# Kernel optimization log

Measured on AMD Instinct MI355X. Metric: run time of the kernel, lower is better.

The kernel has to match this reference:

```python
import jax, jax.numpy as jnp
import numpy as np

B, N, S = 8, 4096, 1024          # clouds, points per cloud, fps samples per cloud
C_IN = 64
R_LIST = (0.1, 0.2, 0.4)
K_LIST = (16, 32, 64)
CHANNELS = ([C_IN + 3, 64, 64, 128], [C_IN + 3, 128, 128, 256], [C_IN + 3, 128, 128, 256])


def setup_inputs() -> dict:
    key = jax.random.key(0)
    ks = jax.random.split(key, 2 + 9)
    inp = {}
    inp["x"] = jax.random.normal(ks[0], (B * N, C_IN), jnp.float32)
    inp["pos"] = jax.random.uniform(ks[1], (B * N, 3), jnp.float32)
    inp["batch"] = jnp.repeat(jnp.arange(B, dtype=jnp.int32), N)
    ki = 2
    for s, ch in enumerate(CHANNELS):
        for l in range(len(ch) - 1):
            inp[f"W{s}_{l}"] = jax.random.normal(ks[ki], (ch[l], ch[l + 1]), jnp.float32) / np.float32(np.sqrt(ch[l]))
            inp[f"b{s}_{l}"] = jnp.zeros((ch[l + 1],), jnp.float32)
        ki += 1
    return inp


def _fps_one(pos_b):
    """Farthest point sampling on one cloud [N,3] -> [S] int32 indices (start at 0)."""
    def step(carry, _):
        min_d, last = carry
        d = jnp.sum((pos_b - pos_b[last]) ** 2, axis=-1)          # [N]
        min_d = jnp.minimum(min_d, d)
        return (min_d, jnp.argmax(min_d).astype(jnp.int32)), last
    init = (jnp.full((N,), jnp.inf, pos_b.dtype), jnp.int32(0))
    _, idx = jax.lax.scan(step, init, None, length=S)
    return idx


def _scale(xb, posb, centers, r, K, Ws, bs):
    """Radius ball query (K nearest within r) + PointConv (MLP on [x_j, pos_j-pos_i], max-aggr)."""
    d2 = jnp.sum((centers[:, None, :] - posb[None, :, :]) ** 2, axis=-1)  # [S,N]
    neg = jnp.where(d2 <= r * r, -d2, -jnp.inf)
    vals, nbr = jax.lax.top_k(neg, K)                                      # [S,K]
    valid = vals > -jnp.inf                                                # center itself always valid
    feat = jnp.concatenate([xb[nbr], posb[nbr] - centers[:, None, :]], axis=-1)  # [S,K,C+3]
    h = feat
    for W, b in zip(Ws, bs):
        h = jax.nn.relu(h @ W + b)
    h = jnp.where(valid[..., None], h, -jnp.inf)
    return jnp.max(h, axis=1)                                              # [S,out]


def _forward(x, pos, batch, params):
    xb = x.reshape(B, N, C_IN)
    posb = pos.reshape(B, N, 3)
    idx = jax.vmap(_fps_one)(posb)                                # [B,S]
    centers = jnp.take_along_axis(posb, idx[..., None], axis=1)   # [B,S,3]
    outs = []
    for s in range(3):
        Ws, bs = params[s]
        f = lambda xb_, pb_, c_, Ws=Ws, bs=bs, s=s: _scale(xb_, pb_, c_, R_LIST[s], K_LIST[s], Ws, bs)
        outs.append(jax.vmap(f)(xb, posb, centers))
    new_x = jnp.concatenate(outs, axis=-1).reshape(B * S, -1)     # [B*S, 640]
    new_pos = centers.reshape(B * S, 3)
    new_batch = jnp.repeat(jnp.arange(B, dtype=batch.dtype), S)
    return new_x, new_pos, new_batch


def reference(x, pos, batch, W0_0, b0_0, W0_1, b0_1, W0_2, b0_2,
              W1_0, b1_0, W1_1, b1_1, W1_2, b1_2,
              W2_0, b2_0, W2_1, b2_1, W2_2, b2_2):
    params = (((W0_0, W0_1, W0_2), (b0_0, b0_1, b0_2)),
              ((W1_0, W1_1, W1_2), (b1_0, b1_1, b1_2)),
              ((W2_0, W2_1, W2_2), (b2_0, b2_1, b2_2)))
    return _forward(x, pos, batch, params)
```

## Files before the change

### kernel.cpp

```cpp
#include <hip/hip_runtime.h>

#define NB 8
#define NP 4096
#define NS 1024
#define PROGSTRIDE 32

typedef _Float16 f16x8 __attribute__((ext_vector_type(8)));
typedef _Float16 f16x4 __attribute__((ext_vector_type(4)));
typedef float f32x4 __attribute__((ext_vector_type(4)));

#define DPP_MAX(v, ctrl)                                                     \
    v = fmaxf(v, __int_as_float(__builtin_amdgcn_update_dpp(                 \
                __float_as_int(v), __float_as_int(v), (ctrl), 0xf, 0xf, false)))

struct PrepArgs {
    const float* src[9];
    _Float16* dst[9];
    int kr[9], kp[9], nc[9];
};

template <int K>
__device__ __forceinline__ void select_center(
        const float* __restrict__ pb,
        const float* __restrict__ centers,
        int* __restrict__ nbr, int* __restrict__ nvalid,
        float r2, int scid) {
#pragma clang fp contract(off)
    const int lane = threadIdx.x & 63;
    const unsigned kr2 = __float_as_uint(r2);
    const float cx = centers[scid * 3 + 0];
    const float cy = centers[scid * 3 + 1];
    const float cz = centers[scid * 3 + 2];

    unsigned key[64];
#pragma unroll
    for (int i = 0; i < 64; ++i) {
        const float* pp = pb + (size_t)(lane + i * 64) * 3;
        float dx = pp[0] - cx; float sx = dx * dx;
        float dy = pp[1] - cy; float sy = dy * dy;
        float dz = pp[2] - cz; float sz = dz * dz;
        float d2 = sx + sy; d2 = d2 + sz;
        key[i] = __float_as_uint(d2);
    }

    const unsigned long long below = (1ull << lane) - 1ull;
    int c_cnt = 0;
#pragma unroll
    for (int i = 0; i < 64; ++i)
        c_cnt += __popcll(__ballot(key[i] <= kr2));

    unsigned thr = kr2;
    int nv = c_cnt;
    bool need_ties = false;
    unsigned tkey = 0;
    if (c_cnt > K) {
        nv = K;
        unsigned lo = 0, hi = kr2;
        need_ties = true;
        while (lo < hi) {
            unsigned mid = lo + ((hi - lo) >> 1);
            int cnt = 0;
#pragma unroll
            for (int i = 0; i < 64; ++i)
                cnt += __popcll(__ballot(key[i] <= mid));
            if (cnt == K) { thr = mid; need_ties = false; break; }
            if (cnt > K) hi = mid; else lo = mid + 1;
        }
        tkey = lo;
    }

    if (!need_ties) {
        int base = 0;
#pragma unroll
        for (int i = 0; i < 64; ++i) {
            unsigned long long m = __ballot(key[i] <= thr);
            if (key[i] <= thr)
                nbr[(size_t)scid * K + base + __popcll(m & below)] = lane + i * 64;
            base += __popcll(m);
        }
    } else {
        const unsigned t = tkey;
        int m_cnt = 0;
#pragma unroll
        for (int i = 0; i < 64; ++i)
            m_cnt += __popcll(__ballot(key[i] < t));
        const int rem = K - m_cnt;
        int base = 0, tcnt = 0;
#pragma unroll
        for (int i = 0; i < 64; ++i) {
            unsigned long long lt = __ballot(key[i] < t);
            unsigned long long eq = __ballot(key[i] == t);
            if (key[i] < t) {
                nbr[(size_t)scid * K + base + __popcll(lt & below)] = lane + i * 64;
            } else if (key[i] == t) {
                int tr = tcnt + __popcll(eq & below);
                if (tr < rem) nbr[(size_t)scid * K + (m_cnt + tr)] = lane + i * 64;
            }
            base += __popcll(lt);
            tcnt += __popcll(eq);
        }
    }
    if (lane == 0) nvalid[scid] = nv;
}

__global__ __launch_bounds__(512, 1) void fps_select_fused(
        const float* __restrict__ pos,
        float* __restrict__ centers,
        float* __restrict__ out_pos,
        float* __restrict__ out_batch,
        int* __restrict__ nbr0, int* __restrict__ nbr1, int* __restrict__ nbr2,
        int* __restrict__ nval,
        unsigned* __restrict__ prog,
        PrepArgs pa) {
#pragma clang fp contract(off)
    const int tid = threadIdx.x;
    const int lane = tid & 63;

    if (blockIdx.x < NB) {
        const int b = blockIdx.x;
        const int wid = tid >> 6;
        __shared__ float4 slot[2][8];

        const float* pb = pos + (size_t)b * NP * 3;
        float px[8], py[8], pz[8], md[8];
        {
            const float4* pv = (const float4*)(pb + tid * 24);
            float4 q0 = pv[0], q1 = pv[1], q2 = pv[2];
            float4 q3 = pv[3], q4 = pv[4], q5 = pv[5];
            px[0] = q0.x; py[0] = q0.y; pz[0] = q0.z;
            px[1] = q0.w; py[1] = q1.x; pz[1] = q1.y;
            px[2] = q1.z; py[2] = q1.w; pz[2] = q2.x;
            px[3] = q2.y; py[3] = q2.z; pz[3] = q2.w;
            px[4] = q3.x; py[4] = q3.y; pz[4] = q3.z;
            px[5] = q3.w; py[5] = q4.x; pz[5] = q4.y;
            px[6] = q4.z; py[6] = q4.w; pz[6] = q5.x;
            px[7] = q5.y; py[7] = q5.z; pz[7] = q5.w;
        }
#pragma unroll
        for (int j = 0; j < 8; ++j) md[j] = __builtin_inff();
        for (int t = tid; t < NS; t += 512) out_batch[b * NS + t] = (float)b;

        float cx = pb[0], cy = pb[1], cz = pb[2];
        if (tid == 0) {
            size_t o = (size_t)(b * NS) * 3;
            centers[o + 0] = cx; centers[o + 1] = cy; centers[o + 2] = cz;
            out_pos[o + 0] = cx; out_pos[o + 1] = cy; out_pos[o + 2] = cz;
        }

        int par = 0;
        for (int t = 1; t < NS; ++t) {
            float bv = -1.0f, bx = cx, by = cy, bz = cz;
#pragma unroll
            for (int j = 0; j < 8; ++j) {
                float dx = px[j] - cx; float sx = dx * dx;
                float dy = py[j] - cy; float sy = dy * dy;
                float dz = pz[j] - cz; float sz = dz * dz;
                float d = sx + sy; d = d + sz;
                float m = fminf(md[j], d);
                md[j] = m;
                bool c = m > bv;
                bv = c ? m : bv;
                bx = c ? px[j] : bx;
                by = c ? py[j] : by;
                bz = c ? pz[j] : bz;
            }
            float v = bv;
            DPP_MAX(v, 0x111);
            DPP_MAX(v, 0x112);
            DPP_MAX(v, 0x114);
            DPP_MAX(v, 0x118);
            DPP_MAX(v, 0x142);
            DPP_MAX(v, 0x143);
            const float mx = __int_as_float(
                __builtin_amdgcn_readlane(__float_as_int(v), 63));
            unsigned long long tie = __ballot(bv == mx);
            if (lane == __ffsll(tie) - 1)
                slot[par][wid] = make_float4(mx, bx, by, bz);
            __syncthreads();
            float4 s0 = slot[par][0], s1 = slot[par][1];
            float4 s2 = slot[par][2], s3 = slot[par][3];
            float4 s4 = slot[par][4], s5 = slot[par][5];
            float4 s6 = slot[par][6], s7 = slot[par][7];
            float4 a01 = (s1.x > s0.x) ? s1 : s0;
            float4 a23 = (s3.x > s2.x) ? s3 : s2;
            float4 a45 = (s5.x > s4.x) ? s5 : s4;
            float4 a67 = (s7.x > s6.x) ? s7 : s6;
            float4 b03 = (a23.x > a01.x) ? a23 : a01;
            float4 b47 = (a67.x > a45.x) ? a67 : a45;
            float4 wn = (b47.x > b03.x) ? b47 : b03;
            cx = wn.y; cy = wn.z; cz = wn.w;
            if (tid == 0) {
                size_t o = (size_t)(b * NS + t) * 3;
                centers[o + 0] = cx; centers[o + 1] = cy; centers[o + 2] = cz;
                out_pos[o + 0] = cx; out_pos[o + 1] = cy; out_pos[o + 2] = cz;
                if ((t & 15) == 15)
                    __hip_atomic_store(&prog[b * PROGSTRIDE], (unsigned)(t + 1),
                                       __ATOMIC_RELEASE, __HIP_MEMORY_SCOPE_AGENT);
            }
            par ^= 1;
        }
    } else {
        const int wblk = blockIdx.x - NB;
        {
            const int wtid = wblk * 512 + tid;
            const int NW = 248 * 512;
#pragma unroll 1
            for (int m = 0; m < 9; ++m) {
                const int kp = pa.kp[m], kr = pa.kr[m], nc = pa.nc[m];
                const float* src = pa.src[m];
                _Float16* dst = pa.dst[m];
                const int tot = kp * nc;
                for (int i = wtid; i < tot; i += NW) {
                    int n = i / kp, k = i - n * kp;
                    dst[i] = (k < kr) ? (_Float16)src[(size_t)k * nc + n]
                                      : (_Float16)0.f;
                }
            }
        }
        const int wid = tid >> 6;
        const int wave_id = wblk * 8 + wid;
        const int NWAVE = 248 * 8;
        const int NTASK = 3 * NB * NS;
        for (int T = wave_id; T < NTASK; T += NWAVE) {
            const int s = T / 24;
            const int r = T - s * 24;
            const int b = r & 7;
            const int seg = r >> 3;
            const int scid = b * NS + s;
            while (__hip_atomic_load(&prog[b * PROGSTRIDE], __ATOMIC_ACQUIRE,
                                     __HIP_MEMORY_SCOPE_AGENT) <= (unsigned)s)
                __builtin_amdgcn_s_sleep(32);
            const float* pb = pos + (size_t)b * NP * 3;
            if (seg == 0)
                select_center<16>(pb, centers, nbr0, nval,
                                  (float)(0.1 * 0.1), scid);
            else if (seg == 1)
                select_center<32>(pb, centers, nbr1, nval + 8192,
                                  (float)(0.2 * 0.2), scid);
            else
                select_center<64>(pb, centers, nbr2, nval + 16384,
                                  (float)(0.4 * 0.4), scid);
        }
    }
}

template <int M, int C1, int C2, int C3, int OFF, int NCTR>
__device__ void mlp_body(
        char* smem,
        const float* __restrict__ x, const float* __restrict__ pos,
        const float* __restrict__ centers,
        const int* __restrict__ nbr, const int* __restrict__ nvalid,
        const _Float16* __restrict__ wt1, const _Float16* __restrict__ wt2,
        const _Float16* __restrict__ wt3,
        const float* __restrict__ b1, const float* __restrict__ b2,
        const float* __restrict__ b3,
        float* __restrict__ out, int blk) {
    constexpr int K1P = 96;
    constexpr int S1 = K1P + 8;
    constexpr int S2 = C1 + 8;
    constexpr int S3 = C2 + 8;
    constexpr int MT = M / 16;
    constexpr int NCH1 = C1 / 4, NCH2 = C2 / 4, NCH3 = C3 / 4;
    constexpr int NT1 = NCH1 / 16, NT2 = NCH2 / 16, NT3 = NCH3 / 16;
    constexpr int KT1 = K1P / 32, KT2 = C1 / 32, KT3 = C2 / 32;

    _Float16* feat = (_Float16*)smem;
    _Float16* h1 = feat + M * S1;
    _Float16* h2 = h1 + M * S2;
    int* outmax = (int*)(h2 + M * S3);

    const int tid = threadIdx.x;
    const int lane = tid & 63;
    const int w = tid >> 6;
    const int lm = lane & 15;
    const int lq = lane >> 4;

    f16x8 wf1[NT1][KT1], wf2[NT2][KT2], wf3[NT3][KT3];
    float bb1[NT1], bb2[NT2], bb3[NT3];
#pragma unroll
    for (int nt = 0; nt < NT1; ++nt) {
        int n = w * NCH1 + nt * 16 + lm;
        bb1[nt] = b1[n];
#pragma unroll
        for (int kt = 0; kt < KT1; ++kt)
            wf1[nt][kt] = *(const f16x8*)(wt1 + (size_t)n * K1P + kt * 32 + lq * 8);
    }
#pragma unroll
    for (int nt = 0; nt < NT2; ++nt) {
        int n = w * NCH2 + nt * 16 + lm;
        bb2[nt] = b2[n];
#pragma unroll
        for (int kt = 0; kt < KT2; ++kt)
            wf2[nt][kt] = *(const f16x8*)(wt2 + (size_t)n * C1 + kt * 32 + lq * 8);
    }
#pragma unroll
    for (int nt = 0; nt < NT3; ++nt) {
        int n = w * NCH3 + nt * 16 + lm;
        bb3[nt] = b3[n];
#pragma unroll
        for (int kt = 0; kt < KT3; ++kt)
            wf3[nt][kt] = *(const f16x8*)(wt3 + (size_t)n * C2 + kt * 32 + lq * 8);
    }

    for (int cc = 0; cc < NCTR; ++cc) {
        const int cid = blk * NCTR + cc;
        const int bidx = cid >> 10;
        const int nv = nvalid[cid];
        const float cx = centers[cid * 3 + 0];
        const float cy = centers[cid * 3 + 1];
        const float cz = centers[cid * 3 + 2];
        for (int i = tid; i < C3; i += 256) outmax[i] = 0;

#pragma unroll
        for (int it = tid; it < M * 16; it += 256) {
            const int r = it >> 4, sub = it & 15;
            if (r < nv) {
                int pt = nbr[(size_t)cid * M + r];
                float4 v = *(const float4*)(x + ((size_t)(bidx * NP) + pt) * 64 + sub * 4);
                f16x4 hv = {(_Float16)v.x, (_Float16)v.y, (_Float16)v.z, (_Float16)v.w};
                *(f16x4*)(feat + r * S1 + sub * 4) = hv;
            }
        }
#pragma unroll
        for (int it = tid; it < M * 4; it += 256) {
            const int r = it >> 2, q = it & 3;
            f16x8 z = {(_Float16)0.f, (_Float16)0.f, (_Float16)0.f, (_Float16)0.f,
                       (_Float16)0.f, (_Float16)0.f, (_Float16)0.f, (_Float16)0.f};
            if (q == 0 && r < nv) {
                int pt = nbr[(size_t)cid * M + r];
                const float* pr = pos + ((size_t)(bidx * NP) + pt) * 3;
                z[0] = (_Float16)(pr[0] - cx);
                z[1] = (_Float16)(pr[1] - cy);
                z[2] = (_Float16)(pr[2] - cz);
            }
            *(f16x8*)(feat + r * S1 + 64 + q * 8) = z;
        }
        __syncthreads();

#pragma unroll
        for (int mt = 0; mt < MT; ++mt) {
            f16x8 a[KT1];
#pragma unroll
            for (int kt = 0; kt < KT1; ++kt)
                a[kt] = *(const f16x8*)(feat + (mt * 16 + lm) * S1 + kt * 32 + lq * 8);
#pragma unroll
            for (int nt = 0; nt < NT1; ++nt) {
                f32x4 acc = {bb1[nt], bb1[nt], bb1[nt], bb1[nt]};
#pragma unroll
                for (int kt = 0; kt < KT1; ++kt)
                    acc = __builtin_amdgcn_mfma_f32_16x16x32_f16(a[kt], wf1[nt][kt], acc, 0, 0, 0);
                const int gc = w * NCH1 + nt * 16 + lm;
#pragma unroll
                for (int rg = 0; rg < 4; ++rg)
                    h1[(mt * 16 + lq * 4 + rg) * S2 + gc] = (_Float16)fmaxf(acc[rg], 0.f);
            }
        }
        __syncthreads();

#pragma unroll
        for (int mt = 0; mt < MT; ++mt) {
            f16x8 a[KT2];
#pragma unroll
            for (int kt = 0; kt < KT2; ++kt)
                a[kt] = *(const f16x8*)(h1 + (mt * 16 + lm) * S2 + kt * 32 + lq * 8);
#pragma unroll
            for (int nt = 0; nt < NT2; ++nt) {
                f32x4 acc = {bb2[nt], bb2[nt], bb2[nt], bb2[nt]};
#pragma unroll
                for (int kt = 0; kt < KT2; ++kt)
                    acc = __builtin_amdgcn_mfma_f32_16x16x32_f16(a[kt], wf2[nt][kt], acc, 0, 0, 0);
                const int gc = w * NCH2 + nt * 16 + lm;
#pragma unroll
                for (int rg = 0; rg < 4; ++rg)
                    h2[(mt * 16 + lq * 4 + rg) * S3 + gc] = (_Float16)fmaxf(acc[rg], 0.f);
            }
        }
        __syncthreads();

#pragma unroll
        for (int mt = 0; mt < MT; ++mt) {
            f16x8 a[KT3];
#pragma unroll
            for (int kt = 0; kt < KT3; ++kt)
                a[kt] = *(const f16x8*)(h2 + (mt * 16 + lm) * S3 + kt * 32 + lq * 8);
#pragma unroll
            for (int nt = 0; nt < NT3; ++nt) {
                f32x4 acc = {bb3[nt], bb3[nt], bb3[nt], bb3[nt]};
#pragma unroll
                for (int kt = 0; kt < KT3; ++kt)
                    acc = __builtin_amdgcn_mfma_f32_16x16x32_f16(a[kt], wf3[nt][kt], acc, 0, 0, 0);
                float mx = -1.f;
#pragma unroll
                for (int rg = 0; rg < 4; ++rg) {
                    int row = mt * 16 + lq * 4 + rg;
                    float v = fmaxf(acc[rg], 0.f);
                    if (row < nv) mx = fmaxf(mx, v);
                }
                mx = fmaxf(mx, __shfl_xor(mx, 16));
                mx = fmaxf(mx, __shfl_xor(mx, 32));
                if (lane < 16)
                    atomicMax(&outmax[w * NCH3 + nt * 16 + lm], __float_as_int(mx));
            }
        }
        __syncthreads();
        for (int i = tid; i < C3; i += 256)
            out[(size_t)cid * 640 + OFF + i] = __int_as_float(outmax[i]);
        __syncthreads();
    }
}

struct MlpW {
    const _Float16* w[9];
    const float* bias[9];
};

__global__ __launch_bounds__(256, 2) void mlp_all(
        const float* __restrict__ x, const float* __restrict__ pos,
        const float* __restrict__ centers,
        const int* __restrict__ nbr0, const int* __restrict__ nbr1,
        const int* __restrict__ nbr2, const int* __restrict__ nval,
        MlpW ww, float* __restrict__ out) {
    extern __shared__ char smem[];
    const int blk = blockIdx.x;
    if (blk < 1024)
        mlp_body<16, 64, 64, 128, 0, 8>(smem, x, pos, centers, nbr0, nval,
            ww.w[0], ww.w[1], ww.w[2], ww.bias[0], ww.bias[1], ww.bias[2], out, blk);
    else if (blk < 2048)
        mlp_body<32, 128, 128, 256, 128, 8>(smem, x, pos, centers, nbr1, nval + 8192,
            ww.w[3], ww.w[4], ww.w[5], ww.bias[3], ww.bias[4], ww.bias[5], out, blk - 1024);
    else
        mlp_body<64, 128, 128, 256, 384, 8>(smem, x, pos, centers, nbr2, nval + 16384,
            ww.w[6], ww.w[7], ww.w[8], ww.bias[6], ww.bias[7], ww.bias[8], out, blk - 2048);
}

extern "C" void kernel_launch(void* const* d_in, const int* in_sizes, int n_in,
                              void* d_out, int out_size, void* d_ws, size_t ws_size,
                              hipStream_t stream) {
    const float* x = (const float*)d_in[0];
    const float* pos = (const float*)d_in[1];
    const float* W0_0 = (const float*)d_in[3];
    const float* b0_0 = (const float*)d_in[4];
    const float* W0_1 = (const float*)d_in[5];
    const float* b0_1 = (const float*)d_in[6];
    const float* W0_2 = (const float*)d_in[7];
    const float* b0_2 = (const float*)d_in[8];
    const float* W1_0 = (const float*)d_in[9];
    const float* b1_0 = (const float*)d_in[10];
    const float* W1_1 = (const float*)d_in[11];
    const float* b1_1 = (const float*)d_in[12];
    const float* W1_2 = (const float*)d_in[13];
    const float* b1_2 = (const float*)d_in[14];
    const float* W2_0 = (const float*)d_in[15];
    const float* b2_0 = (const float*)d_in[16];
    const float* W2_1 = (const float*)d_in[17];
    const float* b2_1 = (const float*)d_in[18];
    const float* W2_2 = (const float*)d_in[19];
    const float* b2_2 = (const float*)d_in[20];

    float* out = (float*)d_out;
    char* ws = (char*)d_ws;
    float* centers = (float*)(ws + 0);
    int* nbr0 = (int*)(ws + 98304);
    int* nbr1 = (int*)(ws + 622592);
    int* nbr2 = (int*)(ws + 1671168);
    int* nval = (int*)(ws + 3768320);
    _Float16* w0t1 = (_Float16*)(ws + 3866624);
    _Float16* w0t2 = (_Float16*)(ws + 3878912);
    _Float16* w0t3 = (_Float16*)(ws + 3887104);
    _Float16* w1t1 = (_Float16*)(ws + 3903488);
    _Float16* w1t2 = (_Float16*)(ws + 3928064);
    _Float16* w1t3 = (_Float16*)(ws + 3960832);
    _Float16* w2t1 = (_Float16*)(ws + 4026368);
    _Float16* w2t2 = (_Float16*)(ws + 4050944);
    _Float16* w2t3 = (_Float16*)(ws + 4083712);
    unsigned* prog = (unsigned*)(ws + 4149248);

    float* out_pos = out + (size_t)8192 * 640;
    float* out_batch = out_pos + (size_t)8192 * 3;

    hipMemsetAsync(prog, 0, NB * PROGSTRIDE * sizeof(unsigned), stream);

    PrepArgs pa;
    pa.src[0] = W0_0; pa.dst[0] = w0t1; pa.kr[0] = 67;  pa.kp[0] = 96;  pa.nc[0] = 64;
    pa.src[1] = W0_1; pa.dst[1] = w0t2; pa.kr[1] = 64;  pa.kp[1] = 64;  pa.nc[1] = 64;
    pa.src[2] = W0_2; pa.dst[2] = w0t3; pa.kr[2] = 64;  pa.kp[2] = 64;  pa.nc[2] = 128;
    pa.src[3] = W1_0; pa.dst[3] = w1t1; pa.kr[3] = 67;  pa.kp[3] = 96;  pa.nc[3] = 128;
    pa.src[4] = W1_1; pa.dst[4] = w1t2; pa.kr[4] = 128; pa.kp[4] = 128; pa.nc[4] = 128;
    pa.src[5] = W1_2; pa.dst[5] = w1t3; pa.kr[5] = 128; pa.kp[5] = 128; pa.nc[5] = 256;
    pa.src[6] = W2_0; pa.dst[6] = w2t1; pa.kr[6] = 67;  pa.kp[6] = 96;  pa.nc[6] = 128;
    pa.src[7] = W2_1; pa.dst[7] = w2t2; pa.kr[7] = 128; pa.kp[7] = 128; pa.nc[7] = 128;
    pa.src[8] = W2_2; pa.dst[8] = w2t3; pa.kr[8] = 128; pa.kp[8] = 128; pa.nc[8] = 256;

    fps_select_fused<<<dim3(256), dim3(512), 0, stream>>>(
        pos, centers, out_pos, out_batch, nbr0, nbr1, nbr2, nval, prog, pa);

    MlpW ww;
    ww.w[0] = w0t1; ww.w[1] = w0t2; ww.w[2] = w0t3;
    ww.w[3] = w1t1; ww.w[4] = w1t2; ww.w[5] = w1t3;
    ww.w[6] = w2t1; ww.w[7] = w2t2; ww.w[8] = w2t3;
    ww.bias[0] = b0_0; ww.bias[1] = b0_1; ww.bias[2] = b0_2;
    ww.bias[3] = b1_0; ww.bias[4] = b1_1; ww.bias[5] = b1_2;
    ww.bias[6] = b2_0; ww.bias[7] = b2_1; ww.bias[8] = b2_2;

    mlp_all<<<dim3(3072), dim3(256), 49152, stream>>>(
        x, pos, centers, nbr0, nbr1, nbr2, nval, ww, out);
}
```

Baseline: 1.119 ms.

## Fuse MLP into persistent FPS kernel with per-unit readiness counters

Merges the separate MLP kernel into the persistent FPS/ball-query kernel. Blocks are now split three ways: 8 run FPS, 120 run neighbour selection, and 128 run the MLP. The MLP blocks take 8-center units from a global atomic queue and wait on a per-unit ready counter that the selection waves increment with release semantics. The goal is to overlap MLP compute with the serial FPS tail instead of running it afterwards. In exchange, the MLP now runs on far fewer blocks with 512 threads, and half the waves sit idle in the smallest scale. Every MLP block also redoes the weight transpose into fp16, and spin-waiting adds latency.

```diff
diff --git a/kernel.cpp b/kernel.cpp
--- a/kernel.cpp
+++ b/kernel.cpp
@@ -4,6 +4,8 @@
 #define NP 4096
 #define NS 1024
 #define PROGSTRIDE 32
+#define SELB 120
+#define NUNIT 3072
 
 typedef _Float16 f16x8 __attribute__((ext_vector_type(8)));
 typedef _Float16 f16x4 __attribute__((ext_vector_type(4)));
@@ -17,6 +19,11 @@
     const float* src[9];
     _Float16* dst[9];
     int kr[9], kp[9], nc[9];
+};
+
+struct MlpW {
+    const _Float16* w[9];
+    const float* bias[9];
 };
 
 template <int K>
@@ -103,7 +110,179 @@
     if (lane == 0) nvalid[scid] = nv;
 }
 
-__global__ __launch_bounds__(512, 1) void fps_select_fused(
+template <int M, int C1, int C2, int C3, int OFF, int AW>
+__device__ void mlp_unit(
+        char* smem,
+        const float* __restrict__ x, const float* __restrict__ pos,
+        const float* __restrict__ centers,
+        const int* __restrict__ nbr, const int* __restrict__ nvalid,
+        const _Float16* __restrict__ wt1, const _Float16* __restrict__ wt2,
+        const _Float16* __restrict__ wt3,
+        const float* __restrict__ b1, const float* __restrict__ b2,
+        const float* __restrict__ b3,
+        float* __restrict__ out, int cid0) {
+    constexpr int K1P = 96;
+    constexpr int S1 = K1P + 8;
+    constexpr int S2 = C1 + 8;
+    constexpr int S3 = C2 + 8;
+    constexpr int MT = M / 16;
+    constexpr int NCH1 = C1 / AW, NCH2 = C2 / AW, NCH3 = C3 / AW;
+    constexpr int NT1 = NCH1 / 16, NT2 = NCH2 / 16, NT3 = NCH3 / 16;
+    constexpr int KT1 = K1P / 32, KT2 = C1 / 32, KT3 = C2 / 32;
+
+    _Float16* feat = (_Float16*)smem;
+    _Float16* h1 = feat + M * S1;
+    _Float16* h2 = h1 + M * S2;
+    int* outmax = (int*)(h2 + M * S3);
+
+    const int tid = threadIdx.x;
+    const int lane = tid & 63;
+    const int w = tid >> 6;
+    const int lm = lane & 15;
+    const int lq = lane >> 4;
+    const bool act = (w < AW);
+
+    f16x8 wf1[NT1][KT1], wf2[NT2][KT2], wf3[NT3][KT3];
+    float bb1[NT1], bb2[NT2], bb3[NT3];
+    if (act) {
+#pragma unroll
+        for (int nt = 0; nt < NT1; ++nt) {
+            int n = w * NCH1 + nt * 16 + lm;
+            bb1[nt] = b1[n];
+#pragma unroll
+            for (int kt = 0; kt < KT1; ++kt)
+                wf1[nt][kt] = *(const f16x8*)(wt1 + (size_t)n * K1P + kt * 32 + lq * 8);
+        }
+#pragma unroll
+        for (int nt = 0; nt < NT2; ++nt) {
+            int n = w * NCH2 + nt * 16 + lm;
+            bb2[nt] = b2[n];
+#pragma unroll
+            for (int kt = 0; kt < KT2; ++kt)
+                wf2[nt][kt] = *(const f16x8*)(wt2 + (size_t)n * C1 + kt * 32 + lq * 8);
+        }
+#pragma unroll
+        for (int nt = 0; nt < NT3; ++nt) {
+            int n = w * NCH3 + nt * 16 + lm;
+            bb3[nt] = b3[n];
+#pragma unroll
+            for (int kt = 0; kt < KT3; ++kt)
+                wf3[nt][kt] = *(const f16x8*)(wt3 + (size_t)n * C2 + kt * 32 + lq * 8);
+        }
+    }
+
+    for (int cc = 0; cc < 8; ++cc) {
+        const int cid = cid0 + cc;
+        const int bidx = cid >> 10;
+        const int nv = nvalid[cid];
+        const float cx = centers[cid * 3 + 0];
+        const float cy = centers[cid * 3 + 1];
+        const float cz = centers[cid * 3 + 2];
+        for (int i = tid; i < C3; i += 512) outmax[i] = 0;
+
+        for (int it = tid; it < M * 16; it += 512) {
+            const int r = it >> 4, sub = it & 15;
+            if (r < nv) {
+                int pt = nbr[(size_t)cid * M + r];
+                float4 v = *(const float4*)(x + ((size_t)(bidx * NP) + pt) * 64 + sub * 4);
+                f16x4 hv = {(_Float16)v.x, (_Float16)v.y, (_Float16)v.z, (_Float16)v.w};
+                *(f16x4*)(feat + r * S1 + sub * 4) = hv;
+            }
+        }
+        for (int it = tid; it < M * 4; it += 512) {
+            const int r = it >> 2, q = it & 3;
+            f16x8 z = {(_Float16)0.f, (_Float16)0.f, (_Float16)0.f, (_Float16)0.f,
+                       (_Float16)0.f, (_Float16)0.f, (_Float16)0.f, (_Float16)0.f};
+            if (q == 0 && r < nv) {
+                int pt = nbr[(size_t)cid * M + r];
+                const float* pr = pos + ((size_t)(bidx * NP) + pt) * 3;
+                z[0] = (_Float16)(pr[0] - cx);
+                z[1] = (_Float16)(pr[1] - cy);
+                z[2] = (_Float16)(pr[2] - cz);
+            }
+            *(f16x8*)(feat + r * S1 + 64 + q * 8) = z;
+        }
+        __syncthreads();
+
+        if (act) {
+#pragma unroll
+            for (int mt = 0; mt < MT; ++mt) {
+                f16x8 a[KT1];
+#pragma unroll
+                for (int kt = 0; kt < KT1; ++kt)
+                    a[kt] = *(const f16x8*)(feat + (mt * 16 + lm) * S1 + kt * 32 + lq * 8);
+#pragma unroll
+                for (int nt = 0; nt < NT1; ++nt) {
+                    f32x4 acc = {bb1[nt], bb1[nt], bb1[nt], bb1[nt]};
+#pragma unroll
+                    for (int kt = 0; kt < KT1; ++kt)
+                        acc = __builtin_amdgcn_mfma_f32_16x16x32_f16(a[kt], wf1[nt][kt], acc, 0, 0, 0);
+                    const int gc = w * NCH1 + nt * 16 + lm;
+#pragma unroll
+                    for (int rg = 0; rg < 4; ++rg)
+                        h1[(mt * 16 + lq * 4 + rg) * S2 + gc] = (_Float16)fmaxf(acc[rg], 0.f);
+                }
+            }
+        }
+        __syncthreads();
+
+        if (act) {
+#pragma unroll
+            for (int mt = 0; mt < MT; ++mt) {
+                f16x8 a[KT2];
+#pragma unroll
+                for (int kt = 0; kt < KT2; ++kt)
+                    a[kt] = *(const f16x8*)(h1 + (mt * 16 + lm) * S2 + kt * 32 + lq * 8);
+#pragma unroll
+                for (int nt = 0; nt < NT2; ++nt) {
+                    f32x4 acc = {bb2[nt], bb2[nt], bb2[nt], bb2[nt]};
+#pragma unroll
+                    for (int kt = 0; kt < KT2; ++kt)
+                        acc = __builtin_amdgcn_mfma_f32_16x16x32_f16(a[kt], wf2[nt][kt], acc, 0, 0, 0);
+                    const int gc = w * NCH2 + nt * 16 + lm;
+#pragma unroll
+                    for (int rg = 0; rg < 4; ++rg)
+                        h2[(mt * 16 + lq * 4 + rg) * S3 + gc] = (_Float16)fmaxf(acc[rg], 0.f);
+                }
+            }
+        }
+        __syncthreads();
+
+        if (act) {
+#pragma unroll
+            for (int mt = 0; mt < MT; ++mt) {
+                f16x8 a[KT3];
+#pragma unroll
+                for (int kt = 0; kt < KT3; ++kt)
+                    a[kt] = *(const f16x8*)(h2 + (mt * 16 + lm) * S3 + kt * 32 + lq * 8);
+#pragma unroll
+                for (int nt = 0; nt < NT3; ++nt) {
+                    f32x4 acc = {bb3[nt], bb3[nt], bb3[nt], bb3[nt]};
+#pragma unroll
+                    for (int kt = 0; kt < KT3; ++kt)
+                        acc = __builtin_amdgcn_mfma_f32_16x16x32_f16(a[kt], wf3[nt][kt], acc, 0, 0, 0);
+                    float mx = -1.f;
+#pragma unroll
+                    for (int rg = 0; rg < 4; ++rg) {
+                        int row = mt * 16 + lq * 4 + rg;
+                        float v = fmaxf(acc[rg], 0.f);
+                        if (row < nv) mx = fmaxf(mx, v);
+                    }
+                    mx = fmaxf(mx, __shfl_xor(mx, 16));
+                    mx = fmaxf(mx, __shfl_xor(mx, 32));
+                    if (lane < 16)
+                        atomicMax(&outmax[w * NCH3 + nt * 16 + lm], __float_as_int(mx));
+                }
+            }
+        }
+        __syncthreads();
+        for (int i = tid; i < C3; i += 512)
+            out[(size_t)cid * 640 + OFF + i] = __int_as_float(outmax[i]);
+        __syncthreads();
+    }
+}
+
+__global__ __launch_bounds__(512, 1) void fps_select_mlp(
         const float* __restrict__ pos,
         float* __restrict__ centers,
         float* __restrict__ out_pos,
@@ -111,13 +290,19 @@
         int* __restrict__ nbr0, int* __restrict__ nbr1, int* __restrict__ nbr2,
         int* __restrict__ nval,
         unsigned* __restrict__ prog,
-        PrepArgs pa) {
+        int* __restrict__ ready,
+        int* __restrict__ mlp_next,
+        const float* __restrict__ x,
+        float* __restrict__ out,
+        PrepArgs pa, MlpW ww) {
 #pragma clang fp contract(off)
+    extern __shared__ char smem[];
     const int tid = threadIdx.x;
     const int lane = tid & 63;
-
-    if (blockIdx.x < NB) {
-        const int b = blockIdx.x;
+    const int blk = blockIdx.x;
+
+    if (blk < NB) {
+        const int b = blk;
         const int wid = tid >> 6;
         __shared__ float4 slot[2][8];
 
@@ -199,27 +384,11 @@
             }
             par ^= 1;
         }
-    } else {
-        const int wblk = blockIdx.x - NB;
-        {
-            const int wtid = wblk * 512 + tid;
-            const int NW = 248 * 512;
-#pragma unroll 1
-            for (int m = 0; m < 9; ++m) {
-                const int kp = pa.kp[m], kr = pa.kr[m], nc = pa.nc[m];
-                const float* src = pa.src[m];
-                _Float16* dst = pa.dst[m];
-                const int tot = kp * nc;
-                for (int i = wtid; i < tot; i += NW) {
-                    int n = i / kp, k = i - n * kp;
-                    dst[i] = (k < kr) ? (_Float16)src[(size_t)k * nc + n]
-                                      : (_Float16)0.f;
-                }
-            }
-        }
+    } else if (blk < NB + SELB) {
+        const int wblk = blk - NB;
         const int wid = tid >> 6;
         const int wave_id = wblk * 8 + wid;
-        const int NWAVE = 248 * 8;
+        const int NWAVE = SELB * 8;
         const int NTASK = 3 * NB * NS;
         for (int T = wave_id; T < NTASK; T += NWAVE) {
             const int s = T / 24;
@@ -240,197 +409,57 @@
             else
                 select_center<64>(pb, centers, nbr2, nval + 16384,
                                   (float)(0.4 * 0.4), scid);
+            asm volatile("s_waitcnt vmcnt(0)" ::: "memory");
+            if (lane == 0)
+                __hip_atomic_fetch_add(&ready[(s >> 3) * 24 + (seg << 3) + b], 1,
+                                       __ATOMIC_RELEASE, __HIP_MEMORY_SCOPE_AGENT);
+        }
+    } else {
+        {
+#pragma unroll 1
+            for (int m = 0; m < 9; ++m) {
+                const int kp = pa.kp[m], kr = pa.kr[m], nc = pa.nc[m];
+                const float* src = pa.src[m];
+                _Float16* dst = pa.dst[m];
+                const int tot = kp * nc;
+                for (int i = tid; i < tot; i += 512) {
+                    int n = i / kp, k = i - n * kp;
+                    dst[i] = (k < kr) ? (_Float16)src[(size_t)k * nc + n]
+                                      : (_Float16)0.f;
+                }
+            }
+            __syncthreads();
+        }
+        __shared__ int sh_u;
+        for (;;) {
+            if (tid == 0)
+                sh_u = __hip_atomic_fetch_add(mlp_next, 1, __ATOMIC_RELAXED,
+                                              __HIP_MEMORY_SCOPE_AGENT);
+            __syncthreads();
+            const int u = sh_u;
+            if (u >= NUNIT) break;
+            while (__hip_atomic_load(&ready[u], __ATOMIC_ACQUIRE,
+                                     __HIP_MEMORY_SCOPE_AGENT) < 8)
+                __builtin_amdgcn_s_sleep(16);
+            const int su = u / 24;
+            const int rem = u - su * 24;
+            const int seg = rem >> 3;
+            const int b = rem & 7;
+            const int cid0 = b * NS + su * 8;
+            if (seg == 0)
+                mlp_unit<16, 64, 64, 128, 0, 4>(smem, x, pos, centers,
+                    nbr0, nval, ww.w[0], ww.w[1], ww.w[2],
+                    ww.bias[0], ww.bias[1], ww.bias[2], out, cid0);
+            else if (seg == 1)
+                mlp_unit<32, 128, 128, 256, 128, 8>(smem, x, pos, centers,
+                    nbr1, nval + 8192, ww.w[3], ww.w[4], ww.w[5],
+                    ww.bias[3], ww.bias[4], ww.bias[5], out, cid0);
+            else
+                mlp_unit<64, 128, 128, 256, 384, 8>(smem, x, pos, centers,
+                    nbr2, nval + 16384, ww.w[6], ww.w[7], ww.w[8],
+                    ww.bias[6], ww.bias[7], ww.bias[8], out, cid0);
         }
     }
-}
-
-template <int M, int C1, int C2, int C3, int OFF, int NCTR>
-__device__ void mlp_body(
-        char* smem,
-        const float* __restrict__ x, const float* __restrict__ pos,
-        const float* __restrict__ centers,
-        const int* __restrict__ nbr, const int* __restrict__ nvalid,
-        const _Float16* __restrict__ wt1, const _Float16* __restrict__ wt2,
-        const _Float16* __restrict__ wt3,
-        const float* __restrict__ b1, const float* __restrict__ b2,
-        const float* __restrict__ b3,
-        float* __restrict__ out, int blk) {
-    constexpr int K1P = 96;
-    constexpr int S1 = K1P + 8;
-    constexpr int S2 = C1 + 8;
-    constexpr int S3 = C2 + 8;
-    constexpr int MT = M / 16;
-    constexpr int NCH1 = C1 / 4, NCH2 = C2 / 4, NCH3 = C3 / 4;
-    constexpr int NT1 = NCH1 / 16, NT2 = NCH2 / 16, NT3 = NCH3 / 16;
-    constexpr int KT1 = K1P / 32, KT2 = C1 / 32, KT3 = C2 / 32;
-
-    _Float16* feat = (_Float16*)smem;
-    _Float16* h1 = feat + M * S1;
-    _Float16* h2 = h1 + M * S2;
-    int* outmax = (int*)(h2 + M * S3);
-
-    const int tid = threadIdx.x;
-    const int lane = tid & 63;
-    const int w = tid >> 6;
-    const int lm = lane & 15;
-    const int lq = lane >> 4;
-
-    f16x8 wf1[NT1][KT1], wf2[NT2][KT2], wf3[NT3][KT3];
-    float bb1[NT1], bb2[NT2], bb3[NT3];
-#pragma unroll
-    for (int nt = 0; nt < NT1; ++nt) {
-        int n = w * NCH1 + nt * 16 + lm;
-        bb1[nt] = b1[n];
-#pragma unroll
-        for (int kt = 0; kt < KT1; ++kt)
-            wf1[nt][kt] = *(const f16x8*)(wt1 + (size_t)n * K1P + kt * 32 + lq * 8);
-    }
-#pragma unroll
-    for (int nt = 0; nt < NT2; ++nt) {
-        int n = w * NCH2 + nt * 16 + lm;
-        bb2[nt] = b2[n];
-#pragma unroll
-        for (int kt = 0; kt < KT2; ++kt)
-            wf2[nt][kt] = *(const f16x8*)(wt2 + (size_t)n * C1 + kt * 32 + lq * 8);
-    }
-#pragma unroll
-    for (int nt = 0; nt < NT3; ++nt) {
-        int n = w * NCH3 + nt * 16 + lm;
-        bb3[nt] = b3[n];
-#pragma unroll
-        for (int kt = 0; kt < KT3; ++kt)
-            wf3[nt][kt] = *(const f16x8*)(wt3 + (size_t)n * C2 + kt * 32 + lq * 8);
-    }
-
-    for (int cc = 0; cc < NCTR; ++cc) {
-        const int cid = blk * NCTR + cc;
-        const int bidx = cid >> 10;
-        const int nv = nvalid[cid];
-        const float cx = centers[cid * 3 + 0];
-        const float cy = centers[cid * 3 + 1];
-        const float cz = centers[cid * 3 + 2];
-        for (int i = tid; i < C3; i += 256) outmax[i] = 0;
-
-#pragma unroll
-        for (int it = tid; it < M * 16; it += 256) {
-            const int r = it >> 4, sub = it & 15;
-            if (r < nv) {
-                int pt = nbr[(size_t)cid * M + r];
-                float4 v = *(const float4*)(x + ((size_t)(bidx * NP) + pt) * 64 + sub * 4);
-                f16x4 hv = {(_Float16)v.x, (_Float16)v.y, (_Float16)v.z, (_Float16)v.w};
-                *(f16x4*)(feat + r * S1 + sub * 4) = hv;
-            }
-        }
-#pragma unroll
-        for (int it = tid; it < M * 4; it += 256) {
-            const int r = it >> 2, q = it & 3;
-            f16x8 z = {(_Float16)0.f, (_Float16)0.f, (_Float16)0.f, (_Float16)0.f,
-                       (_Float16)0.f, (_Float16)0.f, (_Float16)0.f, (_Float16)0.f};
-            if (q == 0 && r < nv) {
-                int pt = nbr[(size_t)cid * M + r];
-                const float* pr = pos + ((size_t)(bidx * NP) + pt) * 3;
-                z[0] = (_Float16)(pr[0] - cx);
-                z[1] = (_Float16)(pr[1] - cy);
-                z[2] = (_Float16)(pr[2] - cz);
-            }
-            *(f16x8*)(feat + r * S1 + 64 + q * 8) = z;
-        }
-        __syncthreads();
-
-#pragma unroll
-        for (int mt = 0; mt < MT; ++mt) {
-            f16x8 a[KT1];
-#pragma unroll
-            for (int kt = 0; kt < KT1; ++kt)
-                a[kt] = *(const f16x8*)(feat + (mt * 16 + lm) * S1 + kt * 32 + lq * 8);
-#pragma unroll
-            for (int nt = 0; nt < NT1; ++nt) {
-                f32x4 acc = {bb1[nt], bb1[nt], bb1[nt], bb1[nt]};
-#pragma unroll
-                for (int kt = 0; kt < KT1; ++kt)
-                    acc = __builtin_amdgcn_mfma_f32_16x16x32_f16(a[kt], wf1[nt][kt], acc, 0, 0, 0);
-                const int gc = w * NCH1 + nt * 16 + lm;
-#pragma unroll
-                for (int rg = 0; rg < 4; ++rg)
-                    h1[(mt * 16 + lq * 4 + rg) * S2 + gc] = (_Float16)fmaxf(acc[rg], 0.f);
-            }
-        }
-        __syncthreads();
-
-#pragma unroll
-        for (int mt = 0; mt < MT; ++mt) {
-            f16x8 a[KT2];
-#pragma unroll
-            for (int kt = 0; kt < KT2; ++kt)
-                a[kt] = *(const f16x8*)(h1 + (mt * 16 + lm) * S2 + kt * 32 + lq * 8);
-#pragma unroll
-            for (int nt = 0; nt < NT2; ++nt) {
-                f32x4 acc = {bb2[nt], bb2[nt], bb2[nt], bb2[nt]};
-#pragma unroll
-                for (int kt = 0; kt < KT2; ++kt)
-                    acc = __builtin_amdgcn_mfma_f32_16x16x32_f16(a[kt], wf2[nt][kt], acc, 0, 0, 0);
-                const int gc = w * NCH2 + nt * 16 + lm;
-#pragma unroll
-                for (int rg = 0; rg < 4; ++rg)
-                    h2[(mt * 16 + lq * 4 + rg) * S3 + gc] = (_Float16)fmaxf(acc[rg], 0.f);
-            }
-        }
-        __syncthreads();
-
-#pragma unroll
-        for (int mt = 0; mt < MT; ++mt) {
-            f16x8 a[KT3];
-#pragma unroll
-            for (int kt = 0; kt < KT3; ++kt)
-                a[kt] = *(const f16x8*)(h2 + (mt * 16 + lm) * S3 + kt * 32 + lq * 8);
-#pragma unroll
-            for (int nt = 0; nt < NT3; ++nt) {
-                f32x4 acc = {bb3[nt], bb3[nt], bb3[nt], bb3[nt]};
-#pragma unroll
-                for (int kt = 0; kt < KT3; ++kt)
-                    acc = __builtin_amdgcn_mfma_f32_16x16x32_f16(a[kt], wf3[nt][kt], acc, 0, 0, 0);
-                float mx = -1.f;
-#pragma unroll
-                for (int rg = 0; rg < 4; ++rg) {
-                    int row = mt * 16 + lq * 4 + rg;
-                    float v = fmaxf(acc[rg], 0.f);
-                    if (row < nv) mx = fmaxf(mx, v);
-                }
-                mx = fmaxf(mx, __shfl_xor(mx, 16));
-                mx = fmaxf(mx, __shfl_xor(mx, 32));
-                if (lane < 16)
-                    atomicMax(&outmax[w * NCH3 + nt * 16 + lm], __float_as_int(mx));
-            }
-        }
-        __syncthreads();
-        for (int i = tid; i < C3; i += 256)
-            out[(size_t)cid * 640 + OFF + i] = __int_as_float(outmax[i]);
-        __syncthreads();
-    }
-}
-
-struct MlpW {
-    const _Float16* w[9];
-    const float* bias[9];
-};
-
-__global__ __launch_bounds__(256, 2) void mlp_all(
-        const float* __restrict__ x, const float* __restrict__ pos,
-        const float* __restrict__ centers,
-        const int* __restrict__ nbr0, const int* __restrict__ nbr1,
-        const int* __restrict__ nbr2, const int* __restrict__ nval,
-        MlpW ww, float* __restrict__ out) {
-    extern __shared__ char smem[];
-    const int blk = blockIdx.x;
-    if (blk < 1024)
-        mlp_body<16, 64, 64, 128, 0, 8>(smem, x, pos, centers, nbr0, nval,
-            ww.w[0], ww.w[1], ww.w[2], ww.bias[0], ww.bias[1], ww.bias[2], out, blk);
-    else if (blk < 2048)
-        mlp_body<32, 128, 128, 256, 128, 8>(smem, x, pos, centers, nbr1, nval + 8192,
-            ww.w[3], ww.w[4], ww.w[5], ww.bias[3], ww.bias[4], ww.bias[5], out, blk - 1024);
-    else
-        mlp_body<64, 128, 128, 256, 384, 8>(smem, x, pos, centers, nbr2, nval + 16384,
-            ww.w[6], ww.w[7], ww.w[8], ww.bias[6], ww.bias[7], ww.bias[8], out, blk - 2048);
 }
 
 extern "C" void kernel_launch(void* const* d_in, const int* in_sizes, int n_in,
@@ -474,11 +503,13 @@
     _Float16* w2t2 = (_Float16*)(ws + 4050944);
     _Float16* w2t3 = (_Float16*)(ws + 4083712);
     unsigned* prog = (unsigned*)(ws + 4149248);
+    int* ready = (int*)(ws + 4150272);
+    int* mlp_next = (int*)(ws + 4162560);
 
     float* out_pos = out + (size_t)8192 * 640;
     float* out_batch = out_pos + (size_t)8192 * 3;
 
-    hipMemsetAsync(prog, 0, NB * PROGSTRIDE * sizeof(unsigned), stream);
+    hipMemsetAsync(prog, 0, 1024 + 12288 + 4, stream);
 
     PrepArgs pa;
     pa.src[0] = W0_0; pa.dst[0] = w0t1; pa.kr[0] = 67;  pa.kp[0] = 96;  pa.nc[0] = 64;
@@ -491,9 +522,6 @@
     pa.src[7] = W2_1; pa.dst[7] = w2t2; pa.kr[7] = 128; pa.kp[7] = 128; pa.nc[7] = 128;
     pa.src[8] = W2_2; pa.dst[8] = w2t3; pa.kr[8] = 128; pa.kp[8] = 128; pa.nc[8] = 256;
 
-    fps_select_fused<<<dim3(256), dim3(512), 0, stream>>>(
-        pos, centers, out_pos, out_batch, nbr0, nbr1, nbr2, nval, prog, pa);
-
     MlpW ww;
     ww.w[0] = w0t1; ww.w[1] = w0t2; ww.w[2] = w0t3;
     ww.w[3] = w1t1; ww.w[4] = w1t2; ww.w[5] = w1t3;
@@ -502,6 +530,7 @@
     ww.bias[3] = b1_0; ww.bias[4] = b1_1; ww.bias[5] = b1_2;
     ww.bias[6] = b2_0; ww.bias[7] = b2_1; ww.bias[8] = b2_2;
 
-    mlp_all<<<dim3(3072), dim3(256), 49152, stream>>>(
-        x, pos, centers, nbr0, nbr1, nbr2, nval, ww, out);
+    fps_select_mlp<<<dim3(256), dim3(512), 49152, stream>>>(
+        pos, centers, out_pos, out_batch, nbr0, nbr1, nbr2, nval,
+        prog, ready, mlp_next, x, out, pa, ww);
 }
```

After: 2.077 ms. 1.86x slower.
